# Kernel optimization log

Hardware: AMD Instinct MI355X
Metric: run time of the kernel (lower is better)

Reference implementation:

```python
import jax, jax.numpy as jnp
import numpy as np

RES = 64
C_DIM = 64
N_BLOCKS = 4
EPS = 1e-12


def conv2d(x, w, b, pad):
    out = jax.lax.conv_general_dilated(
        x, w, window_strides=(1, 1), padding=[(pad, pad), (pad, pad)],
        dimension_numbers=('NCHW', 'OIHW', 'NCHW'))
    return out + b[None, :, None, None]


def unfold3(x):
    # F.unfold(kernel=3, padding=1): [B,C,H,W] -> [B, C*9, H*W], torch ordering (c, ki, kj)
    B, C, H, W = x.shape
    xp = jnp.pad(x, ((0, 0), (0, 0), (1, 1), (1, 1)))
    patches = jnp.stack([xp[:, :, ki:ki + H, kj:kj + W]
                         for ki in range(3) for kj in range(3)], axis=2)  # [B,C,9,H,W]
    return patches.reshape(B, C * 9, H * W)


def fold3(t, H, W):
    # F.fold(kernel=3, padding=1): sum overlapping patches back to [B,C,H,W]
    B, C9, L = t.shape
    C = C9 // 9
    t = t.reshape(B, C, 3, 3, H, W)
    out = jnp.zeros((B, C, H + 2, W + 2), t.dtype)
    for ki in range(3):
        for kj in range(3):
            out = out.at[:, :, ki:ki + H, kj:kj + W].add(t[:, :, ki, kj])
    return out[:, :, 1:H + 1, 1:W + 1]


def setup_inputs() -> dict:
    key = jax.random.key(0)
    ks = jax.random.split(key, 16)
    B, L, C = 4, RES * RES, C_DIM
    s = 0.05
    inp = {
        'c0': jax.random.normal(ks[0], (B, L, C), jnp.float32),
        'f0': jax.random.normal(ks[1], (B, L, C), jnp.float32),
        'c1': jax.random.normal(ks[2], (B, L, C), jnp.float32),
        'head_w': jax.random.normal(ks[3], (C, C, 5, 5), jnp.float32) * s,
        'head_b': jax.random.normal(ks[4], (C,), jnp.float32) * s,
        'rb_w1': jax.random.normal(ks[5], (N_BLOCKS, C, C, 3, 3), jnp.float32) * s,
        'rb_b1': jax.random.normal(ks[6], (N_BLOCKS, C), jnp.float32) * s,
        'rb_w2': jax.random.normal(ks[7], (N_BLOCKS, C, C, 3, 3), jnp.float32) * s,
        'rb_b2': jax.random.normal(ks[8], (N_BLOCKS, C), jnp.float32) * s,
        'tail_w': jax.random.normal(ks[9], (C, C, 5, 5), jnp.float32) * s,
        'tail_b': jax.random.normal(ks[10], (C,), jnp.float32) * s,
        'sq_w': jax.random.normal(ks[11], (C, 2 * C, 5, 5), jnp.float32) * s,
        'sq_b': jax.random.normal(ks[12], (C,), jnp.float32) * s,
    }
    return inp


def reference(c0, f0, c1, head_w, head_b, rb_w1, rb_b1, rb_w2, rb_b2,
              tail_w, tail_b, sq_w, sq_b):
    B, L, C = c1.shape
    H = W = RES
    c1 = c1.swapaxes(1, 2).reshape(B, C, H, W)
    c0 = c0.swapaxes(1, 2).reshape(B, C, H, W)
    f0 = f0.swapaxes(1, 2).reshape(B, C, H, W)
    Delta_c = c1 - c0

    # --- search_Trans: patch correlation + best-match texture transfer ---
    c1u = unfold3(c1)                       # [B, C9, L]
    c0u = unfold3(c0).swapaxes(1, 2)        # [B, L, C9]
    c0n = c0u / jnp.maximum(jnp.linalg.norm(c0u, axis=2, keepdims=True), EPS)
    c1n = c1u / jnp.maximum(jnp.linalg.norm(c1u, axis=1, keepdims=True), EPS)
    R = jnp.einsum('blk,bkm->blm', c0n, c1n)  # [B, L, L]
    R_star = jnp.max(R, axis=1)               # [B, L]
    R_arg = jnp.argmax(R, axis=1)              # [B, L]
    f0u = unfold3(f0)                          # [B, C9, L]
    Tu = jnp.take_along_axis(f0u, R_arg[:, None, :], axis=2)
    T = fold3(Tu, H, W) / 9.0                  # [B, C, H, W]
    S = R_star.reshape(B, 1, H, W)

    # --- residual conv stack on Delta_c ---
    x1 = conv2d(Delta_c, head_w, head_b, 2)
    x = x1
    for i in range(rb_w1.shape[0]):  # NOTE: original feeds x1 into every block
        h = jax.nn.relu(conv2d(x1, rb_w1[i], rb_b1[i], 1))
        x = conv2d(h, rb_w2[i], rb_b2[i], 1) + x1
    x = conv2d(x, tail_w, tail_b, 2)
    Delta_c_fea = x + x1

    x = conv2d(jnp.concatenate([Delta_c_fea, T], axis=1), sq_w, sq_b, 2)
    out = Delta_c_fea + x * S
    return out.reshape(B, C, L).swapaxes(1, 2)
```

## Files before the change

### kernel.cpp

```cpp
#include <hip/hip_runtime.h>
#include <hip/hip_bf16.h>


#define BATCH 4

typedef unsigned short u16;
typedef unsigned int   u32;
typedef __attribute__((ext_vector_type(8))) short short8;
typedef __attribute__((ext_vector_type(4))) float f32x4;

__device__ __forceinline__ void bsplit2(float a, float b, u32& ho, u32& lo) {
  __hip_bfloat16 ha = __float2bfloat16(a), hb = __float2bfloat16(b);
  float ra = a - __bfloat162float(ha), rb = b - __bfloat162float(hb);
  __hip_bfloat16 la = __float2bfloat16(ra), lb = __float2bfloat16(rb);
  ho = (u32)*(u16*)&ha | ((u32)*(u16*)&hb << 16);
  lo = (u32)*(u16*)&la | ((u32)*(u16*)&lb << 16);
}

__device__ __forceinline__ void gload_lds16(const void* g, void* l) {
  __builtin_amdgcn_global_load_lds((const __attribute__((address_space(1))) void*)g,
                                   (__attribute__((address_space(3))) void*)l, 16, 0, 0);
}

__global__ __launch_bounds__(256) void split_pad_kernel(const float* __restrict__ c0,
    const float* __restrict__ c1, u16* __restrict__ p0h, u16* __restrict__ p0l,
    u16* __restrict__ p1h, u16* __restrict__ p1l,
    float* __restrict__ ss0, float* __restrict__ ss1)
{
  int b = blockIdx.y, t = threadIdx.x;
  int pix = blockIdx.x * 4 + (t >> 6);
  int c = t & 63;
  int py = pix / 66, px = pix - py * 66;
  size_t d = ((size_t)b * 4356 + pix) * 64 + c;
  bool interior = (py >= 1 && py <= 64 && px >= 1 && px <= 64);
  float v0 = 0.f, v1 = 0.f;
  if (interior) {
    size_t s = (((size_t)b << 12) + ((py - 1) << 6) + (px - 1)) * 64 + c;
    v0 = c0[s]; v1 = c1[s];
  }
  __hip_bfloat16 h = __float2bfloat16(v0);
  float r = v0 - __bfloat162float(h);
  __hip_bfloat16 lo = __float2bfloat16(r);
  p0h[d] = *(u16*)&h; p0l[d] = *(u16*)&lo;
  h = __float2bfloat16(v1);
  r = v1 - __bfloat162float(h);
  lo = __float2bfloat16(r);
  p1h[d] = *(u16*)&h; p1l[d] = *(u16*)&lo;
  float s0 = v0 * v0, s1 = v1 * v1;
#pragma unroll
  for (int off = 32; off; off >>= 1) {
    s0 += __shfl_xor(s0, off);
    s1 += __shfl_xor(s1, off);
  }
  if (c == 0 && interior) {
    int sstid = (b << 12) + ((py - 1) << 6) + (px - 1);
    ss0[sstid] = s0;
    ss1[sstid] = s1;
  }
}

__global__ __launch_bounds__(256) void wprep_all(
    const float* __restrict__ hw, u16* __restrict__ whh, u16* __restrict__ whl,
    const float* __restrict__ r1, u16* __restrict__ w1h, u16* __restrict__ w1l,
    const float* __restrict__ r2, u16* __restrict__ w2h, u16* __restrict__ w2l,
    const float* __restrict__ tw, u16* __restrict__ wth, u16* __restrict__ wtl,
    const float* __restrict__ sw, u16* __restrict__ wsh, u16* __restrict__ wsl)
{
  int bid = blockIdx.x;
  const float* src; u16 *wh, *wl; int Cin, KK, n, i;
  if (bid < 400)       { src = hw; wh = whh; wl = whl; Cin = 64;  KK = 25; n = 102400; i = bid * 256; }
  else if (bid < 544)  { src = r1; wh = w1h; wl = w1l; Cin = 64;  KK = 9;  n = 36864;  i = (bid - 400) * 256; }
  else if (bid < 688)  { src = r2; wh = w2h; wl = w2l; Cin = 64;  KK = 9;  n = 36864;  i = (bid - 544) * 256; }
  else if (bid < 1088) { src = tw; wh = wth; wl = wtl; Cin = 64;  KK = 25; n = 102400; i = (bid - 688) * 256; }
  else                 { src = sw; wh = wsh; wl = wsl; Cin = 128; KK = 25; n = 204800; i = (bid - 1088) * 256; }
  i += threadIdx.x;
  if (i >= n) return;
  int per = Cin * KK;
  int cout = i / per;
  int rem = i - cout * per;
  int cin = rem / KK;
  int tap = rem - cin * KK;
  float x = src[i];
  __hip_bfloat16 h = __float2bfloat16(x);
  float r = x - __bfloat162float(h);
  __hip_bfloat16 lo = __float2bfloat16(r);
  int d = (tap * 64 + cout) * Cin + cin;
  wh[d] = *(u16*)&h;
  wl[d] = *(u16*)&lo;
}

__global__ __launch_bounds__(256) void corr_mfma(const u16* __restrict__ p0h,
    const u16* __restrict__ p0l, const u16* __restrict__ p1h, const u16* __restrict__ p1l,
    const float* __restrict__ ss0, float* __restrict__ pval, int* __restrict__ pidx)
{
  __shared__ __align__(16) u16 smem[32768];
  __shared__ float linv[512];
  int mt = blockIdx.x, lt = blockIdx.y, b = blockIdx.z;
  int t = threadIdx.x;
  int lane = t & 63, w = t >> 6;
  int wl = w >> 1, wm = w & 1;
  int cc = lane & 15, q = lane >> 4;
  const size_t boff = (size_t)b * 278784;
  const u16* msrc = (w == 0) ? p0h : (w == 1) ? p0l : (w == 2) ? p1h : p1l;
  msrc += boff;
  int isB = w >> 1;

  int srow0 = lane >> 2;
  int cs_g  = (lane & 3) ^ ((lane >> 3) & 3);
  int sw    = (cc >> 1) & 3;

  {
    const float* ssb = ss0 + (b << 12);
    for (int r = t; r < 512; r += 256) {
      int l = (lt << 9) + r;
      int y = l >> 6, x = l & 63;
      float s = 0.f;
      for (int dy = -1; dy <= 1; ++dy) {
        int yy = y + dy; if ((unsigned)yy >= 64u) continue;
        for (int dx = -1; dx <= 1; ++dx) {
          int xx = x + dx; if ((unsigned)xx >= 64u) continue;
          s += ssb[(yy << 6) + xx];
        }
      }
      linv[r] = 1.f / fmaxf(sqrtf(s), 1e-12f);
    }
  }

  const u16* gb[8];
#pragma unroll
  for (int ii = 0; ii < 8; ++ii) {
    int k = (ii << 4) + srow0;
    gb[ii] = msrc + ((((k >> 6) * 66) + (k & 63)) << 6) + (cs_g << 3);
  }

  auto stage = [&](int ssub, int sph, u16* dst) {
    int r = sph >> 1, hh = sph & 1;
    int ki = r / 3, kj = r - ki * 3;
    int pbr = isB ? (mt << 1) : ((lt << 3) + (ssub << 1));
    int uoff = (((pbr + ki) * 66 + kj) << 6) + (hh << 5);
#pragma unroll
    for (int ii = 0; ii < 8; ++ii)
      gload_lds16(gb[ii] + uoff, dst + (ii << 9));
  };

  float bval[4] = {-1e30f, -1e30f, -1e30f, -1e30f};
  int   bidx[4] = {0, 0, 0, 0};

  stage(0, 0, smem + (w << 12));

  for (int sub = 0; sub < 4; ++sub) {
    int row0 = (lt << 9) + (sub << 7);
    f32x4 acc[4][4];
#pragma unroll
    for (int i = 0; i < 4; ++i)
#pragma unroll
      for (int j = 0; j < 4; ++j) acc[i][j] = (f32x4){0.f, 0.f, 0.f, 0.f};

    for (int ph = 0; ph < 18; ++ph) {
      int g = sub * 18 + ph;
      int nxt = g + 1;
      if (nxt < 72) {
        int np = ph + 1, ns = sub;
        if (np == 18) { np = 0; ++ns; }
        stage(ns, np, smem + ((nxt & 1) << 14) + (w << 12));
        asm volatile("s_waitcnt vmcnt(8)" ::: "memory");
      } else {
        asm volatile("s_waitcnt vmcnt(0)" ::: "memory");
      }
      __builtin_amdgcn_s_barrier();
      __builtin_amdgcn_sched_barrier(0);
      const u16* bb = smem + ((g & 1) << 14);
      short8 afh[4], afl[4], bfh[4], bfl[4];
#pragma unroll
      for (int i = 0; i < 4; ++i) {
        int ra = (((wl << 6) + (i << 4) + cc) << 5) + ((q ^ sw) << 3);
        afh[i] = *(const short8*)(&bb[ra]);
        afl[i] = *(const short8*)(&bb[4096 + ra]);
      }
#pragma unroll
      for (int j = 0; j < 4; ++j) {
        int rb = (((wm << 6) + (j << 4) + cc) << 5) + ((q ^ sw) << 3);
        bfh[j] = *(const short8*)(&bb[8192 + rb]);
        bfl[j] = *(const short8*)(&bb[12288 + rb]);
      }
      __builtin_amdgcn_s_setprio(1);
#pragma unroll
      for (int i = 0; i < 4; ++i)
#pragma unroll
        for (int j = 0; j < 4; ++j) {
          acc[i][j] = __builtin_amdgcn_mfma_f32_16x16x32_bf16(afh[i], bfl[j], acc[i][j], 0, 0, 0);
          acc[i][j] = __builtin_amdgcn_mfma_f32_16x16x32_bf16(afl[i], bfh[j], acc[i][j], 0, 0, 0);
          acc[i][j] = __builtin_amdgcn_mfma_f32_16x16x32_bf16(afh[i], bfh[j], acc[i][j], 0, 0, 0);
        }
      __builtin_amdgcn_s_setprio(0);
      __builtin_amdgcn_sched_barrier(0);
      __builtin_amdgcn_s_barrier();
    }
#pragma unroll
    for (int i = 0; i < 4; ++i) {
#pragma unroll
      for (int rg = 0; rg < 4; ++rg) {
        int r = (sub << 7) + (wl << 6) + (i << 4) + (q << 2) + rg;
        float sc = linv[r];
        int l = (lt << 9) + r;
#pragma unroll
        for (int j = 0; j < 4; ++j) {
          float v = acc[i][j][rg] * sc;
          if (v > bval[j]) { bval[j] = v; bidx[j] = l; }
        }
      }
    }
  }

  __syncthreads();
  float* lval = (float*)smem;
  int*   lidx = (int*)((char*)smem + 4096);
  int slot = (wl << 2) + q;
#pragma unroll
  for (int j = 0; j < 4; ++j) {
    int col = (wm << 6) + (j << 4) + cc;
    lval[col * 8 + slot] = bval[j];
    lidx[col * 8 + slot] = bidx[j];
  }
  __syncthreads();
  if (t < 128) {
    float bv = -1e30f; int bi = 0x7FFFFFFF;
    for (int s = 0; s < 8; ++s) {
      float v = lval[t * 8 + s]; int id = lidx[t * 8 + s];
      if (v > bv || (v == bv && id < bi)) { bv = v; bi = id; }
    }
    size_t o = (size_t)(((b << 3) + lt) << 12) + (mt << 7) + t;
    pval[o] = bv; pidx[o] = bi;
  }
}

__global__ __launch_bounds__(256) void tgather_kernel(const float* __restrict__ f0,
    const float* __restrict__ pval, const int* __restrict__ pidx,
    const float* __restrict__ ss1, float* __restrict__ S, float* __restrict__ T)
{
  __shared__ int a3[192];
  int y = blockIdx.x, b = blockIdx.y, t = threadIdx.x;
  if (t < 192) {
    int r = t >> 6, xx = t & 63;
    int yy = y + r - 1;
    bool ok = (yy >= 0 && yy < 64);
    float bv = -1e30f; int bi = 0x7FFFFFFF;
    if (ok) {
      int m = (yy << 6) + xx;
      for (int ltv = 0; ltv < 8; ++ltv) {
        size_t o = (size_t)(((b << 3) + ltv) << 12) + m;
        float v = pval[o]; int id = pidx[o];
        if (v > bv || (v == bv && id < bi)) { bv = v; bi = id; }
      }
      if (r == 1) {
        const float* ssb = ss1 + (b << 12);
        float s = 0.f;
        for (int dy = -1; dy <= 1; ++dy) {
          int y2 = yy + dy; if ((unsigned)y2 >= 64u) continue;
          for (int dx = -1; dx <= 1; ++dx) {
            int x2 = xx + dx; if ((unsigned)x2 >= 64u) continue;
            s += ssb[(y2 << 6) + x2];
          }
        }
        S[(b << 12) + m] = bv / fmaxf(sqrtf(s), 1e-12f);
      }
    }
    a3[t] = (ok && (unsigned)bi < 4096u) ? bi : 0;
  }
  __syncthreads();
  int c = t & 63, pg = t >> 6;
  for (int it = 0; it < 16; ++it) {
    int px = pg + (it << 2);
    float sum = 0.f;
#pragma unroll
    for (int ki = 0; ki < 3; ++ki) {
      int yn = y + 1 - ki;
      if (yn < 0 || yn >= 64) continue;
#pragma unroll
      for (int kj = 0; kj < 3; ++kj) {
        int xn = px + 1 - kj;
        if (xn < 0 || xn >= 64) continue;
        int p = a3[((2 - ki) << 6) + xn];
        int sy = (p >> 6) + ki - 1, sx = (p & 63) + kj - 1;
        if (sy >= 0 && sy < 64 && sx >= 0 && sx < 64)
          sum += f0[((((size_t)b << 12) + (sy << 6) + sx) << 6) + c];
      }
    }
    T[((((size_t)b << 12) + (y << 6) + px)) * 64 + c] = sum * (1.f / 9.f);
  }
}

template<int KS, int CINCH>
__global__ __launch_bounds__(256) void conv_mfma(const float* __restrict__ in0,
    const float* __restrict__ in1, const u16* __restrict__ whp, const u16* __restrict__ wlp,
    const float* __restrict__ bias, float* __restrict__ outp,
    const float* __restrict__ res, const float* __restrict__ smul, int dorelu, int dm)
{
  constexpr int P = KS / 2;
  constexpr int CIN = CINCH * 32;
  constexpr int NKH = CINCH / 2;
  constexpr int NIT = KS * KS * NKH;
  constexpr int AST = 72;
  __shared__ __align__(16) u16 Ah[2][32 * AST], Al[2][32 * AST];
  __shared__ __align__(16) u16 Bh[2][64 * AST], Bl[2][64 * AST];
  int tile = blockIdx.x, b = blockIdx.y;
  int t = threadIdx.x;
  int lane = t & 63, w = t >> 6;
  int wpx = w >> 1, wm = w & 1;
  int cc = lane & 15, q = lane >> 4;
  int ty = tile >> 1, txb = (tile & 1) << 5;
  const size_t abase = (size_t)b << 12;
  f32x4 acc[2];
  acc[0] = (f32x4){0.f, 0.f, 0.f, 0.f};
  acc[1] = (f32x4){0.f, 0.f, 0.f, 0.f};

  uint4 rg[8];
  int arow = t >> 2, acs = t & 3;
  int tb = t - 128;
  int brow = tb >> 1, bhalf = tb & 1;

  auto issue_loads = [&](int itn) {
    int tapn = (NKH == 1) ? itn : (itn >> 1);
    int kh   = (NKH == 1) ? 0 : (itn & 1);
    int ki = tapn / KS, kj = tapn - ki * KS;
    if (t < 128) {
#pragma unroll
      for (int k = 0; k < 8; ++k) rg[k] = make_uint4(0u, 0u, 0u, 0u);
      int iy = ty + ki - P;
      int ix = txb + arow + kj - P;
      if ((unsigned)iy < 64u && (unsigned)ix < 64u) {
        size_t base = (abase + (iy << 6) + ix) << 6;
        int cg = kh * 64 + acs * 16;
        if (dm) {
#pragma unroll
          for (int k = 0; k < 4; ++k) {
            rg[k]     = *(const uint4*)(in0 + base + cg + 4 * k);
            rg[4 + k] = *(const uint4*)(in1 + base + cg + 4 * k);
          }
        } else {
          const float* sp = (CINCH == 4 && kh == 1) ? (in1 + base + (cg - 64))
                                                    : (in0 + base + cg);
#pragma unroll
          for (int k = 0; k < 4; ++k) rg[k] = *(const uint4*)(sp + 4 * k);
        }
      }
    } else {
      size_t so = (size_t)(tapn * 64 + brow) * CIN + kh * 64 + bhalf * 32;
#pragma unroll
      for (int k = 0; k < 4; ++k) {
        rg[k]     = *(const uint4*)&whp[so + 8 * k];
        rg[4 + k] = *(const uint4*)&wlp[so + 8 * k];
      }
    }
  };

  auto write_lds = [&](int cur) {
    if (t < 128) {
      float v[16];
      if (dm) {
#pragma unroll
        for (int k = 0; k < 4; ++k)
#pragma unroll
          for (int e = 0; e < 4; ++e)
            v[k * 4 + e] = __uint_as_float((&rg[4 + k].x)[e]) - __uint_as_float((&rg[k].x)[e]);
      } else {
#pragma unroll
        for (int k = 0; k < 4; ++k)
#pragma unroll
          for (int e = 0; e < 4; ++e)
            v[k * 4 + e] = __uint_as_float((&rg[k].x)[e]);
      }
      uint4 uh0, ul0, uh1, ul1;
      bsplit2(v[0], v[1], uh0.x, ul0.x);
      bsplit2(v[2], v[3], uh0.y, ul0.y);
      bsplit2(v[4], v[5], uh0.z, ul0.z);
      bsplit2(v[6], v[7], uh0.w, ul0.w);
      bsplit2(v[8], v[9], uh1.x, ul1.x);
      bsplit2(v[10], v[11], uh1.y, ul1.y);
      bsplit2(v[12], v[13], uh1.z, ul1.z);
      bsplit2(v[14], v[15], uh1.w, ul1.w);
      int o = arow * AST + acs * 16;
      *(uint4*)&Ah[cur][o]     = uh0;
      *(uint4*)&Ah[cur][o + 8] = uh1;
      *(uint4*)&Al[cur][o]     = ul0;
      *(uint4*)&Al[cur][o + 8] = ul1;
    } else {
      int o = brow * AST + bhalf * 32;
#pragma unroll
      for (int k = 0; k < 4; ++k) {
        *(uint4*)&Bh[cur][o + 8 * k] = rg[k];
        *(uint4*)&Bl[cur][o + 8 * k] = rg[4 + k];
      }
    }
  };

  issue_loads(0);
  for (int it = 0; it < NIT; ++it) {
    int cur = it & 1;
    write_lds(cur);
    if (it + 1 < NIT) issue_loads(it + 1);
    asm volatile("s_waitcnt lgkmcnt(0)" ::: "memory");
    __builtin_amdgcn_s_barrier();
    __builtin_amdgcn_sched_barrier(0);
    short8 afh[2], afl[2], bfh[2][2], bfl[2][2];
#pragma unroll
    for (int ks = 0; ks < 2; ++ks) {
      int ra = ((wpx << 4) + cc) * AST + ks * 32 + (q << 3);
      afh[ks] = *(const short8*)&Ah[cur][ra];
      afl[ks] = *(const short8*)&Al[cur][ra];
#pragma unroll
      for (int j = 0; j < 2; ++j) {
        int rb = ((wm << 5) + (j << 4) + cc) * AST + ks * 32 + (q << 3);
        bfh[j][ks] = *(const short8*)&Bh[cur][rb];
        bfl[j][ks] = *(const short8*)&Bl[cur][rb];
      }
    }
#pragma unroll
    for (int ks = 0; ks < 2; ++ks) {
      acc[0] = __builtin_amdgcn_mfma_f32_16x16x32_bf16(afh[ks], bfl[0][ks], acc[0], 0, 0, 0);
      acc[1] = __builtin_amdgcn_mfma_f32_16x16x32_bf16(afh[ks], bfl[1][ks], acc[1], 0, 0, 0);
      acc[0] = __builtin_amdgcn_mfma_f32_16x16x32_bf16(afl[ks], bfh[0][ks], acc[0], 0, 0, 0);
      acc[1] = __builtin_amdgcn_mfma_f32_16x16x32_bf16(afl[ks], bfh[1][ks], acc[1], 0, 0, 0);
      acc[0] = __builtin_amdgcn_mfma_f32_16x16x32_bf16(afh[ks], bfh[0][ks], acc[0], 0, 0, 0);
      acc[1] = __builtin_amdgcn_mfma_f32_16x16x32_bf16(afh[ks], bfh[1][ks], acc[1], 0, 0, 0);
    }
  }
#pragma unroll
  for (int rgi = 0; rgi < 4; ++rgi) {
    int p = (ty << 6) + txb + (wpx << 4) + (q << 2) + rgi;
#pragma unroll
    for (int j = 0; j < 2; ++j) {
      int cout = (wm << 5) + (j << 4) + cc;
      float v = acc[j][rgi] + bias[cout];
      if (dorelu) v = fmaxf(v, 0.f);
      size_t oi = ((abase + p) << 6) + cout;
      if (smul) v = res[oi] + v * smul[abase + p];
      else if (res) v += res[oi];
      outp[oi] = v;
    }
  }
}

extern "C" void kernel_launch(void* const* d_in, const int* in_sizes, int n_in,
                              void* d_out, int out_size, void* d_ws, size_t ws_size,
                              hipStream_t stream)
{
  (void)in_sizes; (void)n_in; (void)out_size; (void)ws_size;
  const float* c0     = (const float*)d_in[0];
  const float* f0     = (const float*)d_in[1];
  const float* c1     = (const float*)d_in[2];
  const float* head_w = (const float*)d_in[3];
  const float* head_b = (const float*)d_in[4];
  const float* rb_w1  = (const float*)d_in[5];
  const float* rb_b1  = (const float*)d_in[6];
  const float* rb_w2  = (const float*)d_in[7];
  const float* rb_b2  = (const float*)d_in[8];
  const float* tail_w = (const float*)d_in[9];
  const float* tail_b = (const float*)d_in[10];
  const float* sq_w   = (const float*)d_in[11];
  const float* sq_b   = (const float*)d_in[12];
  float* out = (float*)d_out;
  char* ws = (char*)d_ws;

  const size_t OFF_SS0  = 0;
  const size_t OFF_SS1  = 65536;
  const size_t OFF_S    = 262144;
  const size_t OFF_PVAL = 393216;
  const size_t OFF_PIDX = 917504;
  const size_t OFF_WHH  = 1441792;
  const size_t OFF_WHL  = 1646592;
  const size_t OFF_W1H  = 1851392;
  const size_t OFF_W1L  = 1925120;
  const size_t OFF_W2H  = 1998848;
  const size_t OFF_W2L  = 2072576;
  const size_t OFF_WTH  = 2146304;
  const size_t OFF_WTL  = 2351104;
  const size_t OFF_WSH  = 2555904;
  const size_t OFF_WSL  = 2965504;
  const size_t OFF_P0H  = 3375104;
  const size_t OFF_P0L  = OFF_P0H + 2230272;
  const size_t OFF_P1H  = OFF_P0L + 2230272;
  const size_t OFF_P1L  = OFF_P1H + 2230272;
  const size_t OFF_SA   = 3375104;
  const size_t OFF_SB   = 7569408;
  const size_t OFF_SC   = 11763712;

  float* ss0  = (float*)(ws + OFF_SS0);
  float* ss1  = (float*)(ws + OFF_SS1);
  float* Sbuf = (float*)(ws + OFF_S);
  float* pval = (float*)(ws + OFF_PVAL);
  int*   pidx = (int*)(ws + OFF_PIDX);
  u16* whh = (u16*)(ws + OFF_WHH); u16* whl = (u16*)(ws + OFF_WHL);
  u16* w1h = (u16*)(ws + OFF_W1H); u16* w1l = (u16*)(ws + OFF_W1L);
  u16* w2h = (u16*)(ws + OFF_W2H); u16* w2l = (u16*)(ws + OFF_W2L);
  u16* wth = (u16*)(ws + OFF_WTH); u16* wtl = (u16*)(ws + OFF_WTL);
  u16* wsh = (u16*)(ws + OFF_WSH); u16* wsl = (u16*)(ws + OFF_WSL);
  u16* p0h = (u16*)(ws + OFF_P0H); u16* p0l = (u16*)(ws + OFF_P0L);
  u16* p1h = (u16*)(ws + OFF_P1H); u16* p1l = (u16*)(ws + OFF_P1L);
  float* x1  = (float*)(ws + OFF_SA);
  float* Tb  = (float*)(ws + OFF_SA);
  float* hb  = (float*)(ws + OFF_SB);
  float* dcf = (float*)(ws + OFF_SB);
  float* xb  = (float*)(ws + OFF_SC);

  dim3 b256(256);
  split_pad_kernel<<<dim3(1089, BATCH), b256, 0, stream>>>(c0, c1, p0h, p0l, p1h, p1l, ss0, ss1);
  wprep_all<<<dim3(1888), b256, 0, stream>>>(head_w, whh, whl,
      rb_w1 + 110592, w1h, w1l, rb_w2 + 110592, w2h, w2l,
      tail_w, wth, wtl, sq_w, wsh, wsl);

  corr_mfma<<<dim3(32, 8, BATCH), b256, 0, stream>>>(p0h, p0l, p1h, p1l, ss0, pval, pidx);

  dim3 cgrid(128, BATCH);
  conv_mfma<5, 2><<<cgrid, b256, 0, stream>>>(c0, c1, whh, whl, head_b, x1, nullptr, nullptr, 0, 1);
  conv_mfma<3, 2><<<cgrid, b256, 0, stream>>>(x1, nullptr, w1h, w1l, rb_b1 + 192, hb, nullptr, nullptr, 1, 0);
  conv_mfma<3, 2><<<cgrid, b256, 0, stream>>>(hb, nullptr, w2h, w2l, rb_b2 + 192, xb, x1, nullptr, 0, 0);
  conv_mfma<5, 2><<<cgrid, b256, 0, stream>>>(xb, nullptr, wth, wtl, tail_b, dcf, x1, nullptr, 0, 0);

  tgather_kernel<<<dim3(64, BATCH), b256, 0, stream>>>(f0, pval, pidx, ss1, Sbuf, Tb);
  conv_mfma<5, 4><<<cgrid, b256, 0, stream>>>(dcf, Tb, wsh, wsl, sq_b, out, dcf, Sbuf, 0, 0);
}
```

Before: 507.2 us.

## Use 512-thread correlation blocks and precompute inverse patch norms in weight prep

The correlation kernel now runs 8 waves per block instead of 4. Each wave computes a 32x64 output sub-tile rather than 64x64, and pairs of waves share the staging of each operand matrix. The inverse L2 norms of the c0 patches are now computed once in extra blocks of the weight-prep kernel, replacing the recomputation inside every correlation block. This aims to add latency hiding and remove redundant norm work, at the cost of fewer MFMAs per LDS fragment load and more barrier participants.

```diff
diff --git a/kernel.cpp b/kernel.cpp
--- a/kernel.cpp
+++ b/kernel.cpp
@@ -64,9 +64,26 @@
     const float* __restrict__ r1, u16* __restrict__ w1h, u16* __restrict__ w1l,
     const float* __restrict__ r2, u16* __restrict__ w2h, u16* __restrict__ w2l,
     const float* __restrict__ tw, u16* __restrict__ wth, u16* __restrict__ wtl,
-    const float* __restrict__ sw, u16* __restrict__ wsh, u16* __restrict__ wsl)
+    const float* __restrict__ sw, u16* __restrict__ wsh, u16* __restrict__ wsl,
+    const float* __restrict__ ss0, float* __restrict__ inv0)
 {
   int bid = blockIdx.x;
+  if (bid >= 1888) {
+    int tid = (bid - 1888) * 256 + threadIdx.x;
+    int b = tid >> 12, l = tid & 4095;
+    int y = l >> 6, x = l & 63;
+    const float* ssb = ss0 + (b << 12);
+    float s = 0.f;
+    for (int dy = -1; dy <= 1; ++dy) {
+      int yy = y + dy; if ((unsigned)yy >= 64u) continue;
+      for (int dx = -1; dx <= 1; ++dx) {
+        int xx = x + dx; if ((unsigned)xx >= 64u) continue;
+        s += ssb[(yy << 6) + xx];
+      }
+    }
+    inv0[tid] = 1.f / fmaxf(sqrtf(s), 1e-12f);
+    return;
+  }
   const float* src; u16 *wh, *wl; int Cin, KK, n, i;
   if (bid < 400)       { src = hw; wh = whh; wl = whl; Cin = 64;  KK = 25; n = 102400; i = bid * 256; }
   else if (bid < 544)  { src = r1; wh = w1h; wl = w1l; Cin = 64;  KK = 9;  n = 36864;  i = (bid - 400) * 256; }
@@ -89,70 +106,54 @@
   wl[d] = *(u16*)&lo;
 }
 
-__global__ __launch_bounds__(256) void corr_mfma(const u16* __restrict__ p0h,
+__global__ __launch_bounds__(512) void corr_mfma(const u16* __restrict__ p0h,
     const u16* __restrict__ p0l, const u16* __restrict__ p1h, const u16* __restrict__ p1l,
-    const float* __restrict__ ss0, float* __restrict__ pval, int* __restrict__ pidx)
+    const float* __restrict__ inv0, float* __restrict__ pval, int* __restrict__ pidx)
 {
   __shared__ __align__(16) u16 smem[32768];
-  __shared__ float linv[512];
   int mt = blockIdx.x, lt = blockIdx.y, b = blockIdx.z;
   int t = threadIdx.x;
   int lane = t & 63, w = t >> 6;
-  int wl = w >> 1, wm = w & 1;
+  int wa = w >> 1, wm = w & 1;
+  int mat = w >> 1, half = w & 1;
   int cc = lane & 15, q = lane >> 4;
   const size_t boff = (size_t)b * 278784;
-  const u16* msrc = (w == 0) ? p0h : (w == 1) ? p0l : (w == 2) ? p1h : p1l;
+  const u16* msrc = (mat == 0) ? p0h : (mat == 1) ? p0l : (mat == 2) ? p1h : p1l;
   msrc += boff;
-  int isB = w >> 1;
+  const float* inv0b = inv0 + (b << 12);
+  int isB = mat >> 1;
 
   int srow0 = lane >> 2;
   int cs_g  = (lane & 3) ^ ((lane >> 3) & 3);
   int sw    = (cc >> 1) & 3;
 
-  {
-    const float* ssb = ss0 + (b << 12);
-    for (int r = t; r < 512; r += 256) {
-      int l = (lt << 9) + r;
-      int y = l >> 6, x = l & 63;
-      float s = 0.f;
-      for (int dy = -1; dy <= 1; ++dy) {
-        int yy = y + dy; if ((unsigned)yy >= 64u) continue;
-        for (int dx = -1; dx <= 1; ++dx) {
-          int xx = x + dx; if ((unsigned)xx >= 64u) continue;
-          s += ssb[(yy << 6) + xx];
-        }
-      }
-      linv[r] = 1.f / fmaxf(sqrtf(s), 1e-12f);
-    }
-  }
-
-  const u16* gb[8];
-#pragma unroll
-  for (int ii = 0; ii < 8; ++ii) {
-    int k = (ii << 4) + srow0;
+  const u16* gb[4];
+#pragma unroll
+  for (int ii = 0; ii < 4; ++ii) {
+    int k = ((half * 4 + ii) << 4) + srow0;
     gb[ii] = msrc + ((((k >> 6) * 66) + (k & 63)) << 6) + (cs_g << 3);
   }
 
-  auto stage = [&](int ssub, int sph, u16* dst) {
+  auto stage = [&](int ssub, int sph, u16* dstbase) {
     int r = sph >> 1, hh = sph & 1;
     int ki = r / 3, kj = r - ki * 3;
     int pbr = isB ? (mt << 1) : ((lt << 3) + (ssub << 1));
     int uoff = (((pbr + ki) * 66 + kj) << 6) + (hh << 5);
 #pragma unroll
-    for (int ii = 0; ii < 8; ++ii)
-      gload_lds16(gb[ii] + uoff, dst + (ii << 9));
+    for (int ii = 0; ii < 4; ++ii)
+      gload_lds16(gb[ii] + uoff, dstbase + ((half * 4 + ii) << 9));
   };
 
   float bval[4] = {-1e30f, -1e30f, -1e30f, -1e30f};
   int   bidx[4] = {0, 0, 0, 0};
 
-  stage(0, 0, smem + (w << 12));
+  stage(0, 0, smem + (mat << 12));
 
   for (int sub = 0; sub < 4; ++sub) {
     int row0 = (lt << 9) + (sub << 7);
-    f32x4 acc[4][4];
-#pragma unroll
-    for (int i = 0; i < 4; ++i)
+    f32x4 acc[2][4];
+#pragma unroll
+    for (int i = 0; i < 2; ++i)
 #pragma unroll
       for (int j = 0; j < 4; ++j) acc[i][j] = (f32x4){0.f, 0.f, 0.f, 0.f};
 
@@ -162,18 +163,18 @@
       if (nxt < 72) {
         int np = ph + 1, ns = sub;
         if (np == 18) { np = 0; ++ns; }
-        stage(ns, np, smem + ((nxt & 1) << 14) + (w << 12));
-        asm volatile("s_waitcnt vmcnt(8)" ::: "memory");
+        stage(ns, np, smem + ((nxt & 1) << 14) + (mat << 12));
+        asm volatile("s_waitcnt vmcnt(4)" ::: "memory");
       } else {
         asm volatile("s_waitcnt vmcnt(0)" ::: "memory");
       }
       __builtin_amdgcn_s_barrier();
       __builtin_amdgcn_sched_barrier(0);
       const u16* bb = smem + ((g & 1) << 14);
-      short8 afh[4], afl[4], bfh[4], bfl[4];
-#pragma unroll
-      for (int i = 0; i < 4; ++i) {
-        int ra = (((wl << 6) + (i << 4) + cc) << 5) + ((q ^ sw) << 3);
+      short8 afh[2], afl[2], bfh[4], bfl[4];
+#pragma unroll
+      for (int i = 0; i < 2; ++i) {
+        int ra = (((wa << 5) + (i << 4) + cc) << 5) + ((q ^ sw) << 3);
         afh[i] = *(const short8*)(&bb[ra]);
         afl[i] = *(const short8*)(&bb[4096 + ra]);
       }
@@ -185,7 +186,7 @@
       }
       __builtin_amdgcn_s_setprio(1);
 #pragma unroll
-      for (int i = 0; i < 4; ++i)
+      for (int i = 0; i < 2; ++i)
 #pragma unroll
         for (int j = 0; j < 4; ++j) {
           acc[i][j] = __builtin_amdgcn_mfma_f32_16x16x32_bf16(afh[i], bfl[j], acc[i][j], 0, 0, 0);
@@ -197,12 +198,11 @@
       __builtin_amdgcn_s_barrier();
     }
 #pragma unroll
-    for (int i = 0; i < 4; ++i) {
+    for (int i = 0; i < 2; ++i) {
 #pragma unroll
       for (int rg = 0; rg < 4; ++rg) {
-        int r = (sub << 7) + (wl << 6) + (i << 4) + (q << 2) + rg;
-        float sc = linv[r];
-        int l = (lt << 9) + r;
+        int l = row0 + (wa << 5) + (i << 4) + (q << 2) + rg;
+        float sc = inv0b[l];
 #pragma unroll
         for (int j = 0; j < 4; ++j) {
           float v = acc[i][j][rg] * sc;
@@ -214,19 +214,19 @@
 
   __syncthreads();
   float* lval = (float*)smem;
-  int*   lidx = (int*)((char*)smem + 4096);
-  int slot = (wl << 2) + q;
+  int*   lidx = (int*)((char*)smem + 8192);
+  int slot = (wa << 2) + q;
 #pragma unroll
   for (int j = 0; j < 4; ++j) {
     int col = (wm << 6) + (j << 4) + cc;
-    lval[col * 8 + slot] = bval[j];
-    lidx[col * 8 + slot] = bidx[j];
+    lval[col * 16 + slot] = bval[j];
+    lidx[col * 16 + slot] = bidx[j];
   }
   __syncthreads();
   if (t < 128) {
     float bv = -1e30f; int bi = 0x7FFFFFFF;
-    for (int s = 0; s < 8; ++s) {
-      float v = lval[t * 8 + s]; int id = lidx[t * 8 + s];
+    for (int s = 0; s < 16; ++s) {
+      float v = lval[t * 16 + s]; int id = lidx[t * 16 + s];
       if (v > bv || (v == bv && id < bi)) { bv = v; bi = id; }
     }
     size_t o = (size_t)(((b << 3) + lt) << 12) + (mt << 7) + t;
@@ -464,6 +464,7 @@
 
   const size_t OFF_SS0  = 0;
   const size_t OFF_SS1  = 65536;
+  const size_t OFF_INV0 = 131072;
   const size_t OFF_S    = 262144;
   const size_t OFF_PVAL = 393216;
   const size_t OFF_PIDX = 917504;
@@ -487,6 +488,7 @@
 
   float* ss0  = (float*)(ws + OFF_SS0);
   float* ss1  = (float*)(ws + OFF_SS1);
+  float* inv0 = (float*)(ws + OFF_INV0);
   float* Sbuf = (float*)(ws + OFF_S);
   float* pval = (float*)(ws + OFF_PVAL);
   int*   pidx = (int*)(ws + OFF_PIDX);
@@ -505,11 +507,11 @@
 
   dim3 b256(256);
   split_pad_kernel<<<dim3(1089, BATCH), b256, 0, stream>>>(c0, c1, p0h, p0l, p1h, p1l, ss0, ss1);
-  wprep_all<<<dim3(1888), b256, 0, stream>>>(head_w, whh, whl,
+  wprep_all<<<dim3(1952), b256, 0, stream>>>(head_w, whh, whl,
       rb_w1 + 110592, w1h, w1l, rb_w2 + 110592, w2h, w2l,
-      tail_w, wth, wtl, sq_w, wsh, wsl);
-
-  corr_mfma<<<dim3(32, 8, BATCH), b256, 0, stream>>>(p0h, p0l, p1h, p1l, ss0, pval, pidx);
+      tail_w, wth, wtl, sq_w, wsh, wsl, ss0, inv0);
+
+  corr_mfma<<<dim3(32, 8, BATCH), dim3(512), 0, stream>>>(p0h, p0l, p1h, p1l, inv0, pval, pidx);
 
   dim3 cgrid(128, BATCH);
   conv_mfma<5, 2><<<cgrid, b256, 0, stream>>>(c0, c1, whh, whl, head_b, x1, nullptr, nullptr, 0, 1);
```

New measurement: 505.2 us. No clear change (-0.4%).
